# Optimization experiments

Measured on AMD Instinct MI355X. Metric: run time of the kernel, lower is better.

Reference implementation:

```python
import jax, jax.numpy as jnp
import numpy as np
from functools import partial

EPS = 1e-3  # keras LayerNormalization default epsilon

def _conv_same(inp, w):
    # inp: [B,H,W,Cin], w: [k,k,Cin,Cout]
    return jax.lax.conv_general_dilated(
        inp, w, window_strides=(1, 1), padding='SAME',
        dimension_numbers=('NHWC', 'HWIO', 'NHWC'))

def _hard_sigmoid(x):
    # keras recurrent_activation default for ConvLSTM2D
    return jnp.clip(0.2 * x + 0.5, 0.0, 1.0)

def setup_inputs() -> dict:
    key = jax.random.key(0)
    k1, k2, k3 = jax.random.split(key, 3)
    B, T, H, W, C, F, K = 4, 16, 64, 64, 32, 64, 3
    x = jax.random.normal(k1, (B, T, H, W, C), dtype=jnp.float32)
    gamma = jnp.ones((C,), jnp.float32)
    beta = jnp.zeros((C,), jnp.float32)
    # gate order i, f, c, o stacked along output channels (keras convention)
    Wx = jax.random.normal(k2, (K, K, C, 4 * F), dtype=jnp.float32) * 0.05
    Wh = jax.random.normal(k3, (K, K, F, 4 * F), dtype=jnp.float32) * 0.05
    b = jnp.zeros((4 * F,), jnp.float32)
    return {"x": x, "gamma": gamma, "beta": beta, "Wx": Wx, "Wh": Wh, "b": b}

def reference(x, gamma, beta, Wx, Wh, b):
    B, T, H, W, C = x.shape
    F = Wh.shape[2]
    # LayerNorm over channel axis
    mu = jnp.mean(x, axis=-1, keepdims=True)
    var = jnp.var(x, axis=-1, keepdims=True)
    xn = (x - mu) * jax.lax.rsqrt(var + EPS) * gamma + beta

    # Precompute input-to-gate convs for all timesteps at once (time folded into batch)
    zx = _conv_same(xn.reshape(B * T, H, W, C), Wx) + b  # [B*T,H,W,4F]
    zx = zx.reshape(B, T, H, W, 4 * F).transpose(1, 0, 2, 3, 4)  # [T,B,H,W,4F]

    def step(carry, zxt):
        h, c = carry
        z = zxt + _conv_same(h, Wh)
        zi, zf, zc, zo = jnp.split(z, 4, axis=-1)
        i = _hard_sigmoid(zi)
        f = _hard_sigmoid(zf)
        c = f * c + i * jnp.tanh(zc)
        o = _hard_sigmoid(zo)
        h = o * jnp.tanh(c)
        return (h, c), h

    h0 = jnp.zeros((B, H, W, F), x.dtype)
    c0 = jnp.zeros((B, H, W, F), x.dtype)
    _, hs = jax.lax.scan(step, (h0, c0), zx)  # hs: [T,B,H,W,F]
    y = hs.transpose(1, 0, 2, 3, 4)  # [B,T,H,W,F] (return_sequences=True)

    # MaxPool3D pool_size=(1,2,2), stride = pool_size, VALID padding
    y = jax.lax.reduce_window(
        y, -jnp.inf, jax.lax.max,
        window_dimensions=(1, 1, 2, 2, 1),
        window_strides=(1, 1, 2, 2, 1),
        padding='VALID')
    return y
```

## Files before the change

kernel.cpp:

```cpp
#include <hip/hip_runtime.h>
#include <hip/hip_fp16.h>

typedef _Float16 f16;
typedef _Float16 f16x8 __attribute__((ext_vector_type(8)));
typedef float f32x4 __attribute__((ext_vector_type(4)));
typedef unsigned long long ull;

#define BB 4
#define TT 16
#define HH 64
#define WW 64
#define CC 32
#define FF 64
#define GG 256

#define WAITV(n) asm volatile("s_waitcnt vmcnt(" #n ")" ::: "memory")
#define LGKBAR do { asm volatile("s_waitcnt lgkmcnt(0)" ::: "memory"); \
                    __builtin_amdgcn_s_barrier(); \
                    __builtin_amdgcn_sched_barrier(0); } while (0)

__device__ __forceinline__ float hsig(float z) {
    return fminf(fmaxf(0.2f * z + 0.5f, 0.f), 1.f);
}
__device__ __forceinline__ float tanh_fast(float x) {
    return 1.f - 2.f / (__expf(2.f * x) + 1.f);
}

__device__ __forceinline__ void async_copy16(const void* g, void* l) {
    __builtin_amdgcn_global_load_lds(
        (const __attribute__((address_space(1))) unsigned*)g,
        (__attribute__((address_space(3))) unsigned*)l, 16, 0, 0);
}

__global__ void wprep_kernel(const float* __restrict__ wx, const float* __restrict__ wh,
                             f16* __restrict__ wcat) {
    int e = blockIdx.x * 256 + threadIdx.x;
    if (e < 9 * CC * GG) {
        int n = e & 255, k = e >> 8;
        int p = k / 96, r = k % 96;
        wcat[((p * 12 + (r >> 3)) * 256 + n) * 8 + (r & 7)] = (f16)wx[e];
    } else {
        e -= 9 * CC * GG;
        if (e < 9 * FF * GG) {
            int n = e & 255, k = 288 + (e >> 8);
            int p = k / 96, r = k % 96;
            wcat[((p * 12 + (r >> 3)) * 256 + n) * 8 + (r & 7)] = (f16)wh[e];
        }
    }
}

__device__ __forceinline__ void stage_x(const float* __restrict__ x, int bb, int t,
                                        int ty, int tx, int tid,
                                        const float* sg, const float* sb,
                                        f16* __restrict__ xpatch) {
    if (tid < 200) {
        int pix = tid >> 1, part = tid & 1;
        int py = pix / 10, px_ = pix % 10;
        int gy = ty * 8 - 1 + py, gx = tx * 8 - 1 + px_;
        if (gy >= 0 && gy < HH && gx >= 0 && gx < WW) {
            const float* xp = x + ((size_t)(bb * TT + t) * (HH * WW)
                                   + gy * WW + gx) * CC + part * 16;
            float v[16];
            float s = 0.f, s2 = 0.f;
#pragma unroll
            for (int j = 0; j < 4; j++) {
                float4 t4 = *(const float4*)(xp + j * 4);
                v[j * 4] = t4.x; v[j * 4 + 1] = t4.y; v[j * 4 + 2] = t4.z; v[j * 4 + 3] = t4.w;
                s += t4.x + t4.y + t4.z + t4.w;
                s2 += t4.x * t4.x + t4.y * t4.y + t4.z * t4.z + t4.w * t4.w;
            }
            s += __shfl_xor(s, 1);
            s2 += __shfl_xor(s2, 1);
            float mu = s * (1.f / CC);
            float var = s2 * (1.f / CC) - mu * mu;
            float rs = rsqrtf(var + 1e-3f);
            f16 o16[16];
#pragma unroll
            for (int c = 0; c < 16; c++)
                o16[c] = (f16)((v[c] - mu) * rs * sg[part * 16 + c] + sb[part * 16 + c]);
            f16x8* d = (f16x8*)&xpatch[pix * 72 + part * 16];
            d[0] = *(f16x8*)&o16[0];
            d[1] = *(f16x8*)&o16[8];
        }
    }
}

__global__ __launch_bounds__(512, 2)
void fused_kernel(const float* __restrict__ x, const float* __restrict__ gamma,
                  const float* __restrict__ beta, const f16* __restrict__ wcat,
                  const float* __restrict__ bs, f16* __restrict__ halo,
                  float* __restrict__ out, unsigned* __restrict__ flags) {
    __shared__ __align__(16) f16 patches[3 * 7200];
    __shared__ __align__(16) f16 wbuf[6 * 8192];
    __shared__ float sg[CC], sb[CC];

    f16* xpatch = patches;
    int tid = threadIdx.x;
    int tile = blockIdx.x;
    int bb = tile >> 6, ty = (tile >> 3) & 7, tx = tile & 7;
    int lane = tid & 63, w = tid >> 6;
    int wm = w >> 2, nhalf = (w >> 1) & 1, wn = w & 1;
    int quad = lane >> 4, noff = lane & 15;

    if (tid < CC) sg[tid] = gamma[tid];
    else if (tid < 2 * CC) sb[tid - CC] = beta[tid - CC];

    for (int i = tid; i < 2700; i += 512)
        ((f16x8*)patches)[i] = (f16x8){0, 0, 0, 0, 0, 0, 0, 0};

    const char* gwb = (const char*)wcat + w * 2048 + lane * 16;

    int fch = (nhalf << 5) + (wn << 4) + noff;
    float b_i = bs[fch], b_f = bs[64 + fch], b_c = bs[128 + fch], b_o = bs[192 + fch];

    float creg[2][4];
#pragma unroll
    for (int mt = 0; mt < 2; mt++)
#pragma unroll
        for (int r = 0; r < 4; r++) creg[mt][r] = 0.f;

    int mrow[2];
#pragma unroll
    for (int mt = 0; mt < 2; mt++) {
        int m = (wm << 5) + (mt << 4) + noff;
        mrow[mt] = ((m >> 3) * 10 + (m & 7)) * 72 + (quad << 3);
    }
    int rB[4];
#pragma unroll
    for (int cls = 0; cls < 4; cls++) rB[cls] = ((cls << 6) + fch) << 3;

    __syncthreads();

    stage_x(x, bb, 0, ty, tx, tid, sg, sb, xpatch);
#pragma unroll
    for (int k = 0; k < 3; k++) {
        async_copy16(gwb + (size_t)k * 16384, &wbuf[k * 8192 + w * 1024]);
        async_copy16(gwb + (size_t)k * 16384 + 1024, &wbuf[k * 8192 + w * 1024 + 512]);
    }
    WAITV(0);

    for (int t = 0; t < TT; t++) {
        f16* hp_cur = patches + 7200 + (t & 1) * 7200;
        f16* hp_nxt = patches + 7200 + ((t + 1) & 1) * 7200;

        LGKBAR;

        f32x4 acc[2][4];
#pragma unroll
        for (int i = 0; i < 2; i++)
#pragma unroll
            for (int j = 0; j < 4; j++) acc[i][j] = (f32x4){0.f, 0.f, 0.f, 0.f};

        f16x8 fA[2][2], fB[2][4];

        auto READF = [&](int cn) {
            const int pn = cn & 1;
            const bool isx = cn < 9;
            const int hc = cn - 9;
            const int tap = isx ? cn : (hc >> 1);
            const int coff = isx ? 0 : ((hc & 1) << 5);
            const f16* ap = isx ? xpatch : hp_cur;
            const int toff = ((tap / 3) * 10 + (tap % 3)) * 72 + coff;
            fA[pn][0] = *(const f16x8*)&ap[mrow[0] + toff];
            fA[pn][1] = *(const f16x8*)&ap[mrow[1] + toff];
            const f16* wbc = &wbuf[(cn % 6) * 8192 + quad * 2048];
#pragma unroll
            for (int cls = 0; cls < 4; cls++)
                fB[pn][cls] = *(const f16x8*)&wbc[rB[cls]];
        };
        auto MFMA8 = [&](int pc) {
            __builtin_amdgcn_s_setprio(1);
#pragma unroll
            for (int cls = 0; cls < 4; cls++) {
                acc[0][cls] = __builtin_amdgcn_mfma_f32_16x16x32_f16(fA[pc][0], fB[pc][cls], acc[0][cls], 0, 0, 0);
                acc[1][cls] = __builtin_amdgcn_mfma_f32_16x16x32_f16(fA[pc][1], fB[pc][cls], acc[1][cls], 0, 0, 0);
            }
            __builtin_amdgcn_s_setprio(0);
        };

#pragma unroll
        for (int g = 0; g < 9; ++g) {
            if (g > 0) LGKBAR;
            READF(3 * g);
            if (g == 2 && t > 0 && tid >= 256 && tid < 400) {
                int e = tid - 256;
                int hx = e >> 2, quarter = e & 3;
                int py, px_;
                if (hx < 10)      { py = 0; px_ = hx; }
                else if (hx < 20) { py = 9; px_ = hx - 10; }
                else if (hx < 28) { py = 1 + (hx - 20); px_ = 0; }
                else              { py = 1 + (hx - 28); px_ = 9; }
                int gy = ty * 8 - 1 + py, gx = tx * 8 - 1 + px_;
                if (gy >= 0 && gy < HH && gx >= 0 && gx < WW) {
                    int nb = bb * 64 + ((gy >> 3) << 3) + (gx >> 3);
                    while (__hip_atomic_load(&flags[nb], __ATOMIC_RELAXED,
                                             __HIP_MEMORY_SCOPE_AGENT) < (unsigned)t)
                        __builtin_amdgcn_s_sleep(1);
                    const ull* src = (const ull*)(halo + ((size_t)(t * BB + bb) * (HH * WW)
                                                         + gy * WW + gx) * FF) + quarter * 4;
                    f16* dst = &hp_cur[(py * 10 + px_) * 72 + quarter * 16];
#pragma unroll
                    for (int j = 0; j < 4; j++) {
                        ull vv = __hip_atomic_load(src + j, __ATOMIC_RELAXED,
                                                   __HIP_MEMORY_SCOPE_AGENT);
                        *(ull*)(dst + j * 4) = vv;
                    }
                }
            }
            if (g < 8) {
#pragma unroll
                for (int k = 0; k < 3; k++) {
                    int c = 3 * g + 3 + k;
                    async_copy16(gwb + (size_t)c * 16384,
                                 &wbuf[(c % 6) * 8192 + w * 1024]);
                    async_copy16(gwb + (size_t)c * 16384 + 1024,
                                 &wbuf[(c % 6) * 8192 + w * 1024 + 512]);
                }
            }
#pragma unroll
            for (int cw = 0; cw < 3; ++cw) {
                const int c = 3 * g + cw;
                if (cw < 2) READF(c + 1);
                MFMA8(c & 1);
            }
            if (g < 8) WAITV(0);
        }

#pragma unroll
        for (int mt = 0; mt < 2; mt++) {
#pragma unroll
            for (int r = 0; r < 4; r++) {
                int m = (wm << 5) + (mt << 4) + (quad << 2) + r;
                int py8 = m >> 3, px8 = m & 7;
                float zi = acc[mt][0][r] + b_i;
                float zf = acc[mt][1][r] + b_f;
                float zc = acc[mt][2][r] + b_c;
                float zo = acc[mt][3][r] + b_o;
                float ig = hsig(zi), fg = hsig(zf), og = hsig(zo);
                float cn = fg * creg[mt][r] + ig * tanh_fast(zc);
                creg[mt][r] = cn;
                f16 hval = (f16)(og * tanh_fast(cn));
                hp_nxt[((py8 + 1) * 10 + px8 + 1) * 72 + fch] = hval;
                if (py8 == 0 || py8 == 7 || px8 == 0 || px8 == 7) {
                    union { f16 f; unsigned short u; } cvt; cvt.f = hval;
                    unsigned short* hp = (unsigned short*)halo
                        + ((size_t)((t + 1) * BB + bb) * (HH * WW)
                           + (ty * 8 + py8) * WW + (tx * 8 + px8)) * FF + fch;
                    __hip_atomic_store(hp, cvt.u, __ATOMIC_RELAXED, __HIP_MEMORY_SCOPE_AGENT);
                }
            }
        }
        __syncthreads();
        if (tid == 0)
            __hip_atomic_store(&flags[tile], (unsigned)(t + 1), __ATOMIC_RELAXED,
                               __HIP_MEMORY_SCOPE_AGENT);

        {
            int o = tid * 2;
            int f0 = o & 63;
            int ox2 = (o >> 6) & 3, oy2 = (o >> 8) & 3;
            int row = 1 + oy2 * 2, col = 1 + ox2 * 2;
            const f16* hb = &hp_nxt[(row * 10 + col) * 72 + f0];
            float v0 = fmaxf(fmaxf((float)hb[0], (float)hb[72]),
                             fmaxf((float)hb[720], (float)hb[792]));
            float v1 = fmaxf(fmaxf((float)hb[1], (float)hb[73]),
                             fmaxf((float)hb[721], (float)hb[793]));
            size_t ofs = (((size_t)(bb * TT + t) * 32 + (ty * 4 + oy2)) * 32
                          + (tx * 4 + ox2)) * 64 + f0;
            float2 v2; v2.x = v0; v2.y = v1;
            *(float2*)(out + ofs) = v2;
        }

        if (t + 1 < TT) {
#pragma unroll
            for (int k = 0; k < 3; k++) {
                async_copy16(gwb + (size_t)k * 16384, &wbuf[k * 8192 + w * 1024]);
                async_copy16(gwb + (size_t)k * 16384 + 1024, &wbuf[k * 8192 + w * 1024 + 512]);
            }
            stage_x(x, bb, t + 1, ty, tx, tid, sg, sb, xpatch);
            WAITV(0);
        }
    }
}

extern "C" void kernel_launch(void* const* d_in, const int* in_sizes, int n_in,
                              void* d_out, int out_size, void* d_ws, size_t ws_size,
                              hipStream_t stream) {
    const float* x = (const float*)d_in[0];
    const float* gamma = (const float*)d_in[1];
    const float* beta = (const float*)d_in[2];
    const float* wx = (const float*)d_in[3];
    const float* wh = (const float*)d_in[4];
    const float* bs = (const float*)d_in[5];
    float* out = (float*)d_out;

    char* ws = (char*)d_ws;
    f16* wcat = (f16*)(ws + 16777216);
    unsigned* flags = (unsigned*)(ws + 17219584);
    f16* hs = (f16*)(ws + 21413888);

    hipMemsetAsync(flags, 0, 256 * 4, stream);
    wprep_kernel<<<864, 256, 0, stream>>>(wx, wh, wcat);

    fused_kernel<<<256, 512, 0, stream>>>(x, gamma, beta, wcat, bs, hs, out, flags);
}
```

Measured before the change: 258.7 us.

## Keep first six weight chunks in registers and restructure weight streaming pipeline

The weight fragments for the first six K-chunks (x-conv taps 0-5) are now loaded once into registers and reused every timestep, so only 21 of 27 chunks are streamed through LDS per step. The x-tap MFMAs for those chunks run first, the halo exchange moves ahead of the LDS pipeline, and the remaining chunks follow a re-sequenced triple-buffered issue/read/MFMA schedule. This cuts per-step global/LDS weight traffic and barrier count, but adds 96 VGPRs of persistent weight fragments, which may raise register pressure or cause spills and lower occupancy.

```diff
diff --git a/kernel.cpp b/kernel.cpp
--- a/kernel.cpp
+++ b/kernel.cpp
@@ -133,9 +133,24 @@
 
     stage_x(x, bb, 0, ty, tx, tid, sg, sb, xpatch);
 #pragma unroll
-    for (int k = 0; k < 3; k++) {
+    for (int k = 0; k < 6; k++) {
         async_copy16(gwb + (size_t)k * 16384, &wbuf[k * 8192 + w * 1024]);
         async_copy16(gwb + (size_t)k * 16384 + 1024, &wbuf[k * 8192 + w * 1024 + 512]);
+    }
+    WAITV(0);
+    LGKBAR;
+    f16x8 wB[6][4];
+#pragma unroll
+    for (int c = 0; c < 6; c++) {
+        const f16* wbc = &wbuf[c * 8192 + quad * 2048];
+#pragma unroll
+        for (int cls = 0; cls < 4; cls++) wB[c][cls] = *(const f16x8*)&wbc[rB[cls]];
+    }
+    LGKBAR;
+#pragma unroll
+    for (int k = 6; k < 9; k++) {
+        async_copy16(gwb + (size_t)k * 16384, &wbuf[(k - 6) * 8192 + w * 1024]);
+        async_copy16(gwb + (size_t)k * 16384 + 1024, &wbuf[(k - 6) * 8192 + w * 1024 + 512]);
     }
     WAITV(0);
 
@@ -150,6 +165,46 @@
         for (int i = 0; i < 2; i++)
 #pragma unroll
             for (int j = 0; j < 4; j++) acc[i][j] = (f32x4){0.f, 0.f, 0.f, 0.f};
+
+#pragma unroll
+        for (int c = 0; c < 6; c++) {
+            const int toff = ((c / 3) * 10 + (c % 3)) * 72;
+            f16x8 a0 = *(const f16x8*)&xpatch[mrow[0] + toff];
+            f16x8 a1 = *(const f16x8*)&xpatch[mrow[1] + toff];
+            __builtin_amdgcn_s_setprio(1);
+#pragma unroll
+            for (int cls = 0; cls < 4; cls++) {
+                acc[0][cls] = __builtin_amdgcn_mfma_f32_16x16x32_f16(a0, wB[c][cls], acc[0][cls], 0, 0, 0);
+                acc[1][cls] = __builtin_amdgcn_mfma_f32_16x16x32_f16(a1, wB[c][cls], acc[1][cls], 0, 0, 0);
+            }
+            __builtin_amdgcn_s_setprio(0);
+        }
+
+        if (t > 0 && tid >= 256 && tid < 400) {
+            int e = tid - 256;
+            int hx = e >> 2, quarter = e & 3;
+            int py, px_;
+            if (hx < 10)      { py = 0; px_ = hx; }
+            else if (hx < 20) { py = 9; px_ = hx - 10; }
+            else if (hx < 28) { py = 1 + (hx - 20); px_ = 0; }
+            else              { py = 1 + (hx - 28); px_ = 9; }
+            int gy = ty * 8 - 1 + py, gx = tx * 8 - 1 + px_;
+            if (gy >= 0 && gy < HH && gx >= 0 && gx < WW) {
+                int nb = bb * 64 + ((gy >> 3) << 3) + (gx >> 3);
+                while (__hip_atomic_load(&flags[nb], __ATOMIC_RELAXED,
+                                         __HIP_MEMORY_SCOPE_AGENT) < (unsigned)t)
+                    __builtin_amdgcn_s_sleep(1);
+                const ull* src = (const ull*)(halo + ((size_t)(t * BB + bb) * (HH * WW)
+                                                     + gy * WW + gx) * FF) + quarter * 4;
+                f16* dst = &hp_cur[(py * 10 + px_) * 72 + quarter * 16];
+#pragma unroll
+                for (int j = 0; j < 4; j++) {
+                    ull vv = __hip_atomic_load(src + j, __ATOMIC_RELAXED,
+                                               __HIP_MEMORY_SCOPE_AGENT);
+                    *(ull*)(dst + j * 4) = vv;
+                }
+            }
+        }
 
         f16x8 fA[2][2], fB[2][4];
 
@@ -168,7 +223,8 @@
             for (int cls = 0; cls < 4; cls++)
                 fB[pn][cls] = *(const f16x8*)&wbc[rB[cls]];
         };
-        auto MFMA8 = [&](int pc) {
+        auto MFMA8 = [&](int c) {
+            const int pc = c & 1;
             __builtin_amdgcn_s_setprio(1);
 #pragma unroll
             for (int cls = 0; cls < 4; cls++) {
@@ -177,54 +233,34 @@
             }
             __builtin_amdgcn_s_setprio(0);
         };
-
-#pragma unroll
-        for (int g = 0; g < 9; ++g) {
-            if (g > 0) LGKBAR;
-            READF(3 * g);
-            if (g == 2 && t > 0 && tid >= 256 && tid < 400) {
-                int e = tid - 256;
-                int hx = e >> 2, quarter = e & 3;
-                int py, px_;
-                if (hx < 10)      { py = 0; px_ = hx; }
-                else if (hx < 20) { py = 9; px_ = hx - 10; }
-                else if (hx < 28) { py = 1 + (hx - 20); px_ = 0; }
-                else              { py = 1 + (hx - 28); px_ = 9; }
-                int gy = ty * 8 - 1 + py, gx = tx * 8 - 1 + px_;
-                if (gy >= 0 && gy < HH && gx >= 0 && gx < WW) {
-                    int nb = bb * 64 + ((gy >> 3) << 3) + (gx >> 3);
-                    while (__hip_atomic_load(&flags[nb], __ATOMIC_RELAXED,
-                                             __HIP_MEMORY_SCOPE_AGENT) < (unsigned)t)
-                        __builtin_amdgcn_s_sleep(1);
-                    const ull* src = (const ull*)(halo + ((size_t)(t * BB + bb) * (HH * WW)
-                                                         + gy * WW + gx) * FF) + quarter * 4;
-                    f16* dst = &hp_cur[(py * 10 + px_) * 72 + quarter * 16];
-#pragma unroll
-                    for (int j = 0; j < 4; j++) {
-                        ull vv = __hip_atomic_load(src + j, __ATOMIC_RELAXED,
-                                                   __HIP_MEMORY_SCOPE_AGENT);
-                        *(ull*)(dst + j * 4) = vv;
-                    }
-                }
-            }
-            if (g < 8) {
-#pragma unroll
-                for (int k = 0; k < 3; k++) {
-                    int c = 3 * g + 3 + k;
-                    async_copy16(gwb + (size_t)c * 16384,
-                                 &wbuf[(c % 6) * 8192 + w * 1024]);
-                    async_copy16(gwb + (size_t)c * 16384 + 1024,
-                                 &wbuf[(c % 6) * 8192 + w * 1024 + 512]);
-                }
-            }
-#pragma unroll
-            for (int cw = 0; cw < 3; ++cw) {
-                const int c = 3 * g + cw;
-                if (cw < 2) READF(c + 1);
-                MFMA8(c & 1);
-            }
-            if (g < 8) WAITV(0);
-        }
+        auto ISSUE3 = [&](int k0) {
+#pragma unroll
+            for (int k = 0; k < 3; k++) {
+                int c = k0 + k;
+                async_copy16(gwb + (size_t)c * 16384, &wbuf[(c % 6) * 8192 + w * 1024]);
+                async_copy16(gwb + (size_t)c * 16384 + 1024,
+                             &wbuf[(c % 6) * 8192 + w * 1024 + 512]);
+            }
+        };
+
+        LGKBAR;
+        READF(6);
+        ISSUE3(9);
+        READF(7); MFMA8(6);
+        READF(8); MFMA8(7);
+        WAITV(0);
+
+#pragma unroll
+        for (int G = 1; G <= 6; G++) {
+            LGKBAR;
+            READF(6 + 3 * G);
+            MFMA8(5 + 3 * G);
+            if (G < 6) ISSUE3(9 + 3 * G);
+            READF(7 + 3 * G); MFMA8(6 + 3 * G);
+            READF(8 + 3 * G); MFMA8(7 + 3 * G);
+            if (G < 6) WAITV(0);
+        }
+        MFMA8(26);
 
 #pragma unroll
         for (int mt = 0; mt < 2; mt++) {
@@ -272,11 +308,7 @@
         }
 
         if (t + 1 < TT) {
-#pragma unroll
-            for (int k = 0; k < 3; k++) {
-                async_copy16(gwb + (size_t)k * 16384, &wbuf[k * 8192 + w * 1024]);
-                async_copy16(gwb + (size_t)k * 16384 + 1024, &wbuf[k * 8192 + w * 1024 + 512]);
-            }
+            ISSUE3(6);
             stage_x(x, bb, t + 1, ty, tx, tid, sg, sb, xpatch);
             WAITV(0);
         }
```

After: 398.4 us. 1.54x slower.
